# Performance work log

Hardware: AMD Instinct MI355X
Metric: run time of the kernel (lower is better)

## Reference

```python
import jax, jax.numpy as jnp
import numpy as np

N_PTS = 10000
BATCH = 2048          # hypotheses per RANSAC iteration
MAX_ITER = 10
SAMPLE_SIZE = 4       # minimal sample for homography DLT
INL_TH = 2.0          # squared symmetric transfer error threshold
EPS = 1e-8


def normalize_points(pts):
    # kornia.geometry.normalize_points: center + isotropic scale to mean dist sqrt(2)
    mean = pts.mean(axis=1, keepdims=True)                       # [B,1,2]
    d = jnp.linalg.norm(pts - mean, axis=-1).mean(axis=-1)       # [B]
    s = jnp.sqrt(jnp.asarray(2.0, pts.dtype)) / (d + EPS)
    B = pts.shape[0]
    T = jnp.zeros((B, 3, 3), pts.dtype)
    T = T.at[:, 0, 0].set(s).at[:, 1, 1].set(s).at[:, 2, 2].set(1.0)
    T = T.at[:, 0, 2].set(-s * mean[:, 0, 0]).at[:, 1, 2].set(-s * mean[:, 0, 1])
    return (pts - mean) * s[:, None, None], T


def find_homography_dlt(p1, p2):
    # p1,p2: [B,4,2]; weights are all ones -> solve smallest eigvec of A^T A (as kornia does)
    p1n, T1 = normalize_points(p1)
    p2n, T2 = normalize_points(p2)
    x1, y1 = p1n[..., 0], p1n[..., 1]
    x2, y2 = p2n[..., 0], p2n[..., 1]
    o = jnp.ones_like(x1); z = jnp.zeros_like(x1)
    ax = jnp.stack([z, z, z, -x1, -y1, -o, y2 * x1, y2 * y1, y2], -1)
    ay = jnp.stack([x1, y1, o, z, z, z, -x2 * x1, -x2 * y1, -x2], -1)
    A = jnp.concatenate([ax, ay], axis=1)                        # [B,8,9]
    AtA = jnp.einsum('bki,bkj->bij', A, A)                       # [B,9,9]
    _, _, Vh = jnp.linalg.svd(AtA)
    H = Vh[:, -1, :].reshape(-1, 3, 3)                           # smallest singular vector
    H = jnp.linalg.inv(T2) @ (H @ T1)
    return H / (H[:, 2:3, 2:3] + EPS)


def transform_points(H, pts):
    # H: [B,3,3], pts: [N,2] -> [B,N,2] (safe homogeneous division, as kornia)
    ph = jnp.concatenate([pts, jnp.ones_like(pts[..., :1])], -1)  # [N,3]
    pt = jnp.einsum('bij,nj->bni', H, ph)                        # [B,N,3]
    zc = pt[..., 2:3]
    mask = jnp.abs(zc) > EPS
    scale = jnp.where(mask, 1.0 / jnp.where(mask, zc, jnp.ones_like(zc)), jnp.ones_like(zc))
    return pt[..., :2] * scale


def symmetric_transfer_error(p1, p2, H):
    # squared symmetric transfer error (kornia default squared=True)
    Hinv = jnp.linalg.inv(H)
    e1 = ((transform_points(H, p1) - p2[None]) ** 2).sum(-1)
    e2 = ((transform_points(Hinv, p2) - p1[None]) ** 2).sum(-1)
    return e1 + e2                                               # [B,N]


def ransac_forward(kp1, kp2, key):
    n = kp1.shape[0]
    keys = jax.random.split(key, MAX_ITER)
    init = (jnp.asarray(1.0, kp1.dtype), jnp.eye(3, dtype=kp1.dtype), jnp.zeros((n,), bool))

    def body(carry, k):
        best_score, best_model, best_inl = carry
        # batched sampling without replacement: top-k of iid uniforms == randperm[:k]
        u = jax.random.uniform(k, (BATCH, n))
        _, idxs = jax.lax.top_k(u, SAMPLE_SIZE)                  # [BATCH,4] distinct
        H = find_homography_dlt(kp1[idxs], kp2[idxs])            # [BATCH,3,3]
        # remove_bad_models: mask instead of filter (jit-friendly)
        valid = jnp.abs(jnp.diagonal(H, axis1=1, axis2=2)).min(-1) > 1e-6
        err = symmetric_transfer_error(kp1, kp2, H)              # [BATCH,N]
        inl = err <= INL_TH
        scores = jnp.where(valid, inl.sum(-1).astype(kp1.dtype), -1.0)
        bi = jnp.argmax(scores)
        better = scores[bi] > best_score
        best_score = jnp.where(better, scores[bi], best_score)
        best_model = jnp.where(better, H[bi], best_model)
        best_inl = jnp.where(better, inl[bi], best_inl)
        return (best_score, best_model, best_inl), None

    (_, best_model, best_inl), _ = jax.lax.scan(body, init, keys)
    return best_model, best_inl


def setup_inputs():
    key = jax.random.key(0)
    k1, k2 = jax.random.split(key)
    kp1 = jax.random.uniform(k1, (N_PTS, 2), jnp.float32) * 100.0
    kp2 = jax.random.uniform(k2, (N_PTS, 2), jnp.float32) * 100.0
    return {"kp1": kp1, "kp2": kp2}


def reference(kp1, kp2):
    return ransac_forward(kp1, kp2, jax.random.key(42))
```

## Files before the change

### kernel.cpp

```cpp
#include <hip/hip_runtime.h>
#include <stdint.h>

#define JAX_PARTITIONABLE 1

#define N_PTS    10000
#define BATCH    2048
#define MAX_ITER 10
#define NMODELS  (BATCH*MAX_ITER)

#define ROTL(v,d) __builtin_amdgcn_alignbit((v),(v),(uint32_t)(32-(d)))

__device__ __forceinline__ void threefry_rounds(uint32_t k0, uint32_t k1, uint32_t ks2,
                                                uint32_t &x0, uint32_t &x1){
#define TF_R(r) { x0 += x1; x1 = ROTL(x1,(r)); x1 ^= x0; }
  TF_R(13) TF_R(15) TF_R(26) TF_R(6)
  x0 += k1;  x1 += ks2 + 1u;
  TF_R(17) TF_R(29) TF_R(16) TF_R(24)
  x0 += ks2; x1 += k0 + 2u;
  TF_R(13) TF_R(15) TF_R(26) TF_R(6)
  x0 += k0;  x1 += k1 + 3u;
  TF_R(17) TF_R(29) TF_R(16) TF_R(24)
  x0 += k1;  x1 += ks2 + 4u;
  TF_R(13) TF_R(15) TF_R(26) TF_R(6)
  x0 += ks2; x1 += k0 + 5u;
#undef TF_R
}

__device__ __forceinline__ void threefry2x32(uint32_t k0, uint32_t k1, uint32_t &x0, uint32_t &x1){
  const uint32_t ks2 = k0 ^ k1 ^ 0x1BD11BDAu;
  x0 += k0; x1 += k1;
  threefry_rounds(k0, k1, ks2, x0, x1);
}

__device__ __forceinline__ void top4_insert(unsigned long long a[4], unsigned long long key){
  if (key > a[3]){
    if (key > a[0]){ a[3]=a[2]; a[2]=a[1]; a[1]=a[0]; a[0]=key; }
    else if (key > a[1]){ a[3]=a[2]; a[2]=a[1]; a[1]=key; }
    else if (key > a[2]){ a[3]=a[2]; a[2]=key; }
    else { a[3]=key; }
  }
}

__device__ void block_merge_top4(unsigned long long a[4], unsigned long long* sm, int tid){
  sm[tid*4+0]=a[0]; sm[tid*4+1]=a[1]; sm[tid*4+2]=a[2]; sm[tid*4+3]=a[3];
  __syncthreads();
  for (int s = 128; s >= 1; s >>= 1){
    if (tid < s){
      unsigned long long bv[4];
      bv[0]=sm[(tid+s)*4+0]; bv[1]=sm[(tid+s)*4+1]; bv[2]=sm[(tid+s)*4+2]; bv[3]=sm[(tid+s)*4+3];
      unsigned long long ov[4];
      int pa=0, pb=0;
      #pragma unroll
      for (int k=0;k<4;k++){
        unsigned long long va = (pa<4)?a[pa]:0ull;
        unsigned long long vb = (pb<4)?bv[pb]:0ull;
        bool ta = va >= vb;
        ov[k] = ta ? va : vb;
        pa += ta?1:0; pb += ta?0:1;
      }
      a[0]=ov[0]; a[1]=ov[1]; a[2]=ov[2]; a[3]=ov[3];
      sm[tid*4+0]=a[0]; sm[tid*4+1]=a[1]; sm[tid*4+2]=a[2]; sm[tid*4+3]=a[3];
    }
    __syncthreads();
  }
}

__device__ __forceinline__ unsigned int lane_lt_count(unsigned long long m){
  unsigned int c = __builtin_amdgcn_mbcnt_lo((uint32_t)m, 0u);
  return __builtin_amdgcn_mbcnt_hi((uint32_t)(m >> 32), c);
}

#if JAX_PARTITIONABLE
#define TH_BITS 4267479552u
#define WCAP 96

__global__ __launch_bounds__(256) void sample_topk(int* __restrict__ idxs){
  const int b = blockIdx.x;
  const int t = blockIdx.y;
  const int tid = threadIdx.x;
  uint32_t k0 = 0u, k1 = (uint32_t)t;
  threefry2x32(0u, 42u, k0, k1);
  const uint32_t ks2 = k0 ^ k1 ^ 0x1BD11BDAu;

  __shared__ unsigned long long wcand[4*WCAP];
  __shared__ unsigned long long sm[256*4];
  __shared__ unsigned int wcnts[4];

  const unsigned int wbase = (unsigned int)(tid >> 6) * WCAP;
  unsigned int wcnt = 0;

  const uint32_t jb = (uint32_t)(b * N_PTS) + k1;

#define EMIT(u, idx) { \
    unsigned long long mk = __ballot((u) >= TH_BITS); \
    if (mk){ \
      if ((u) >= TH_BITS){ \
        unsigned int slot = wcnt + lane_lt_count(mk); \
        if (slot < WCAP) \
          wcand[wbase + slot] = ((unsigned long long)((u) >> 9) << 32) | (uint32_t)(~(idx)); \
      } \
      wcnt += (unsigned int)__popcll(mk); \
    } }

  uint32_t x1b = jb + (uint32_t)tid;
  for (int iter = 0; iter < 10; ++iter, x1b += 1024u){
    uint32_t a0=k0, a1=k0, a2=k0, a3=k0;
    uint32_t b0=x1b, b1=x1b+256u, b2=x1b+512u, b3=x1b+768u;
#define QR4(r) { a0+=b0; b0=ROTL(b0,r); b0^=a0;  a1+=b1; b1=ROTL(b1,r); b1^=a1; \
                 a2+=b2; b2=ROTL(b2,r); b2^=a2;  a3+=b3; b3=ROTL(b3,r); b3^=a3; }
#define INJ4(p,q) { a0+=(p); b0+=(q); a1+=(p); b1+=(q); a2+=(p); b2+=(q); a3+=(p); b3+=(q); }
    QR4(13) QR4(15) QR4(26) QR4(6)
    INJ4(k1,  ks2 + 1u)
    QR4(17) QR4(29) QR4(16) QR4(24)
    INJ4(ks2, k0 + 2u)
    QR4(13) QR4(15) QR4(26) QR4(6)
    INJ4(k0,  k1 + 3u)
    QR4(17) QR4(29) QR4(16) QR4(24)
    INJ4(k1,  ks2 + 4u)
    QR4(13) QR4(15) QR4(26) QR4(6)
    INJ4(ks2, k0 + 5u)
#undef QR4
#undef INJ4
    uint32_t u0 = a0^b0, u1 = a1^b1, u2 = a2^b2, u3 = a3^b3;
    const uint32_t ibase = (uint32_t)(iter*1024) + (uint32_t)tid;
    if (iter == 9){
      u0 = (ibase        < (uint32_t)N_PTS) ? u0 : 0u;
      u1 = (ibase + 256u < (uint32_t)N_PTS) ? u1 : 0u;
      u2 = (ibase + 512u < (uint32_t)N_PTS) ? u2 : 0u;
      u3 = (ibase + 768u < (uint32_t)N_PTS) ? u3 : 0u;
    }
    EMIT(u0, ibase)
    EMIT(u1, ibase + 256u)
    EMIT(u2, ibase + 512u)
    EMIT(u3, ibase + 768u)
  }
#undef EMIT

  if ((tid & 63) == 0) wcnts[tid >> 6] = wcnt;
  __syncthreads();
  const unsigned int c0 = wcnts[0], c1 = wcnts[1], c2 = wcnts[2], c3 = wcnts[3];
  const unsigned int n = c0 + c1 + c2 + c3;
  const bool good = (n >= 4u) && (c0 <= WCAP) && (c1 <= WCAP) && (c2 <= WCAP) && (c3 <= WCAP);

  unsigned long long a[4] = {0ull,0ull,0ull,0ull};
  if (good){
    #pragma unroll
    for (int w = 0; w < 4; ++w){
      const unsigned int cw = wcnts[w];
      for (unsigned int j = tid; j < cw; j += 256) top4_insert(a, wcand[w*WCAP + j]);
    }
  } else {
    for (int i = tid; i < N_PTS; i += 256){
      uint32_t x0 = k0, x1 = jb + (uint32_t)i;
      threefry_rounds(k0, k1, ks2, x0, x1);
      uint32_t u = x0 ^ x1;
      unsigned long long key = ((unsigned long long)(u >> 9) << 32) | (uint32_t)(~(uint32_t)i);
      top4_insert(a, key);
    }
  }
  block_merge_top4(a, sm, tid);
  if (tid == 0){
    int base = ((t*BATCH)+b)*4;
    idxs[base+0] = (int)(~(uint32_t)(a[0] & 0xffffffffull));
    idxs[base+1] = (int)(~(uint32_t)(a[1] & 0xffffffffull));
    idxs[base+2] = (int)(~(uint32_t)(a[2] & 0xffffffffull));
    idxs[base+3] = (int)(~(uint32_t)(a[3] & 0xffffffffull));
  }
}
#else
__global__ __launch_bounds__(256) void sample_topk(int* __restrict__ idxs){
  const int b = blockIdx.x;
  const int t = blockIdx.y;
  const int tid = threadIdx.x;
  uint32_t k0, k1;
  {
    int i0 = 2*t, i1 = 2*t+1;
    uint32_t u0, u1;
    if (i0 < 10){ u0=(uint32_t)i0; u1=(uint32_t)(i0+10); threefry2x32(0u,42u,u0,u1); k0=u0; }
    else        { u0=(uint32_t)(i0-10); u1=(uint32_t)i0; threefry2x32(0u,42u,u0,u1); k0=u1; }
    if (i1 < 10){ u0=(uint32_t)i1; u1=(uint32_t)(i1+10); threefry2x32(0u,42u,u0,u1); k1=u0; }
    else        { u0=(uint32_t)(i1-10); u1=(uint32_t)i1; threefry2x32(0u,42u,u0,u1); k1=u1; }
  }
  const uint32_t half = 10240000u;
  unsigned long long aLo[4] = {0,0,0,0}, aHi[4] = {0,0,0,0};
  const uint32_t jbase = (uint32_t)(b * N_PTS);
  for (int i = tid; i < N_PTS; i += 256){
    uint32_t x0 = jbase + (uint32_t)i, x1 = x0 + half;
    threefry2x32(k0, k1, x0, x1);
    unsigned long long kLo = ((unsigned long long)(x0 >> 9) << 32) | (uint32_t)(~(uint32_t)i);
    unsigned long long kHi = ((unsigned long long)(x1 >> 9) << 32) | (uint32_t)(~(uint32_t)i);
    top4_insert(aLo, kLo);
    top4_insert(aHi, kHi);
  }
  __shared__ unsigned long long sm[256*4];
  block_merge_top4(aLo, sm, tid);
  if (tid == 0){
    int base = ((t*BATCH)+b)*4;
    for (int s=0;s<4;s++) idxs[base+s] = (int)(~(uint32_t)(aLo[s] & 0xffffffffull));
  }
  __syncthreads();
  block_merge_top4(aHi, sm, tid);
  if (tid == 0){
    int base = ((t*BATCH)+(b+1024))*4;
    for (int s=0;s<4;s++) idxs[base+s] = (int)(~(uint32_t)(aHi[s] & 0xffffffffull));
  }
}
#endif

__global__ __launch_bounds__(64) void dlt_kernel(const float* __restrict__ kp1,
                                                 const float* __restrict__ kp2,
                                                 const int* __restrict__ idxs,
                                                 float* __restrict__ Hout,
                                                 float* __restrict__ Hinvout,
                                                 int* __restrict__ validout){
  const int m = blockIdx.x*64 + threadIdx.x;
  __shared__ double As[64][73];
  double* A = &As[threadIdx.x][0];

  double p1x[4],p1y[4],p2x[4],p2y[4];
  #pragma unroll
  for (int s=0;s<4;s++){
    int id = idxs[m*4+s];
    float2 a = ((const float2*)kp1)[id];
    float2 b = ((const float2*)kp2)[id];
    p1x[s]=a.x; p1y[s]=a.y; p2x[s]=b.x; p2y[s]=b.y;
  }
  double mx1=0,my1=0,mx2=0,my2=0;
  #pragma unroll
  for (int s=0;s<4;s++){ mx1+=p1x[s]; my1+=p1y[s]; mx2+=p2x[s]; my2+=p2y[s]; }
  mx1*=0.25; my1*=0.25; mx2*=0.25; my2*=0.25;
  double d1=0,d2=0;
  #pragma unroll
  for (int s=0;s<4;s++){
    d1 += sqrt((p1x[s]-mx1)*(p1x[s]-mx1) + (p1y[s]-my1)*(p1y[s]-my1));
    d2 += sqrt((p2x[s]-mx2)*(p2x[s]-mx2) + (p2y[s]-my2)*(p2y[s]-my2));
  }
  d1*=0.25; d2*=0.25;
  const double s1 = sqrt(2.0)/(d1 + 1e-8);
  const double s2 = sqrt(2.0)/(d2 + 1e-8);
  #pragma unroll
  for (int s=0;s<4;s++){
    double X1=(p1x[s]-mx1)*s1, Y1=(p1y[s]-my1)*s1;
    double X2=(p2x[s]-mx2)*s2, Y2=(p2y[s]-my2)*s2;
    double* ra = A + s*9;
    ra[0]=0.0; ra[1]=0.0; ra[2]=0.0; ra[3]=-X1; ra[4]=-Y1; ra[5]=-1.0;
    ra[6]=Y2*X1; ra[7]=Y2*Y1; ra[8]=Y2;
    double* rb = A + (4+s)*9;
    rb[0]=X1; rb[1]=Y1; rb[2]=1.0; rb[3]=0.0; rb[4]=0.0; rb[5]=0.0;
    rb[6]=-X2*X1; rb[7]=-X2*Y1; rb[8]=-X2;
  }
  for (int k=0;k<8;k++){
    int piv=k; double pv=fabs(A[k*9+k]);
    for (int r=k+1;r<8;r++){ double v=fabs(A[r*9+k]); if (v>pv){pv=v;piv=r;} }
    if (piv!=k){
      for (int c=k;c<9;c++){ double tmp=A[k*9+c]; A[k*9+c]=A[piv*9+c]; A[piv*9+c]=tmp; }
    }
    double invp = 1.0/A[k*9+k];
    for (int r=k+1;r<8;r++){
      double f = A[r*9+k]*invp;
      for (int c=k+1;c<9;c++) A[r*9+c] -= f*A[k*9+c];
      A[r*9+k]=0.0;
    }
  }
  double h[9];
  h[8]=1.0;
  for (int k=7;k>=0;k--){
    double ssum=0.0;
    for (int c=k+1;c<9;c++) ssum += A[k*9+c]*h[c];
    h[k] = -ssum / A[k*9+k];
  }
  {
    double nn=0.0;
    #pragma unroll
    for (int i=0;i<9;i++) nn += h[i]*h[i];
    double inr = 1.0/sqrt(nn);
    #pragma unroll
    for (int i=0;i<9;i++) h[i]*=inr;
  }
  double M[9];
  #pragma unroll
  for (int r=0;r<3;r++){
    double h0=h[r*3+0], h1=h[r*3+1], h2=h[r*3+2];
    M[r*3+0] = h0*s1;
    M[r*3+1] = h1*s1;
    M[r*3+2] = h0*(-s1*mx1) + h1*(-s1*my1) + h2;
  }
  double Hd[9];
  const double is2 = 1.0/s2;
  #pragma unroll
  for (int c=0;c<3;c++){
    Hd[0*3+c] = M[0*3+c]*is2 + mx2*M[2*3+c];
    Hd[1*3+c] = M[1*3+c]*is2 + my2*M[2*3+c];
    Hd[2*3+c] = M[2*3+c];
  }
  const double dn = 1.0/(Hd[8] + 1e-8);
  #pragma unroll
  for (int i=0;i<9;i++) Hd[i]*=dn;
  float Hf[9];
  #pragma unroll
  for (int i=0;i<9;i++){ Hf[i]=(float)Hd[i]; Hout[m*9+i]=Hf[i]; }
  float mind = fminf(fminf(fabsf(Hf[0]),fabsf(Hf[4])),fabsf(Hf[8]));
  validout[m] = (mind > 1e-6f) ? 1 : 0;
  {
    double a=Hd[0],b=Hd[1],c=Hd[2],d=Hd[3],e=Hd[4],f=Hd[5],g=Hd[6],hh=Hd[7],ii=Hd[8];
    double C00= e*ii-f*hh, C01=-(d*ii-f*g), C02= d*hh-e*g;
    double det = a*C00 + b*C01 + c*C02;
    double idet = 1.0/det;
    double inv[9];
    inv[0]=C00*idet;        inv[1]=(c*hh-b*ii)*idet; inv[2]=(b*f-c*e)*idet;
    inv[3]=C01*idet;        inv[4]=(a*ii-c*g)*idet;  inv[5]=(c*d-a*f)*idet;
    inv[6]=C02*idet;        inv[7]=(b*g-a*hh)*idet;  inv[8]=(a*e-b*d)*idet;
    #pragma unroll
    for (int i=0;i<9;i++) Hinvout[m*9+i]=(float)inv[i];
  }
}

__device__ __forceinline__ int inlier_test(float x1,float y1,float x2,float y2,
                                           const float* __restrict__ H,
                                           const float* __restrict__ Hi){
  float px = __fadd_rn(__fadd_rn(__fmul_rn(H[0],x1), __fmul_rn(H[1],y1)), H[2]);
  float py = __fadd_rn(__fadd_rn(__fmul_rn(H[3],x1), __fmul_rn(H[4],y1)), H[5]);
  float pz = __fadd_rn(__fadd_rn(__fmul_rn(H[6],x1), __fmul_rn(H[7],y1)), H[8]);
  float sc = (fabsf(pz) > 1e-8f) ? __fdiv_rn(1.0f, pz) : 1.0f;
  float dx = __fsub_rn(__fmul_rn(px,sc), x2);
  float dy = __fsub_rn(__fmul_rn(py,sc), y2);
  float e1 = __fadd_rn(__fmul_rn(dx,dx), __fmul_rn(dy,dy));
  if (!(e1 <= 2.0f)) return 0;
  float qx = __fadd_rn(__fadd_rn(__fmul_rn(Hi[0],x2), __fmul_rn(Hi[1],y2)), Hi[2]);
  float qy = __fadd_rn(__fadd_rn(__fmul_rn(Hi[3],x2), __fmul_rn(Hi[4],y2)), Hi[5]);
  float qz = __fadd_rn(__fadd_rn(__fmul_rn(Hi[6],x2), __fmul_rn(Hi[7],y2)), Hi[8]);
  float sc2 = (fabsf(qz) > 1e-8f) ? __fdiv_rn(1.0f, qz) : 1.0f;
  float ex = __fsub_rn(__fmul_rn(qx,sc2), x1);
  float ey = __fsub_rn(__fmul_rn(qy,sc2), y1);
  float e2 = __fadd_rn(__fmul_rn(ex,ex), __fmul_rn(ey,ey));
  float err = __fadd_rn(e1, e2);
  return (err <= 2.0f) ? 1 : 0;
}

#define MODELS_PER_BLOCK 8
__global__ __launch_bounds__(256) void score_kernel(const float* __restrict__ kp1,
                                                    const float* __restrict__ kp2,
                                                    const float* __restrict__ Hall,
                                                    const float* __restrict__ Hinvall,
                                                    const int* __restrict__ validall,
                                                    float* __restrict__ scores){
  const int m0 = blockIdx.x * MODELS_PER_BLOCK;
  const int tid = threadIdx.x;
  __shared__ float sH[MODELS_PER_BLOCK][9], sHi[MODELS_PER_BLOCK][9];
  if (tid < 9*MODELS_PER_BLOCK)        sH [tid/9][tid%9] = Hall[m0*9 + tid];
  else if (tid < 18*MODELS_PER_BLOCK){ int q = tid - 9*MODELS_PER_BLOCK;
                                       sHi[q/9][q%9] = Hinvall[m0*9 + q]; }
  __syncthreads();
  int cnt[MODELS_PER_BLOCK];
  #pragma unroll
  for (int mm=0;mm<MODELS_PER_BLOCK;mm++) cnt[mm]=0;
  for (int i = tid; i < N_PTS; i += 256){
    float2 p1 = ((const float2*)kp1)[i];
    float2 p2 = ((const float2*)kp2)[i];
    #pragma unroll
    for (int mm=0;mm<MODELS_PER_BLOCK;mm++)
      cnt[mm] += inlier_test(p1.x,p1.y,p2.x,p2.y,sH[mm],sHi[mm]);
  }
  __shared__ int wred[4][MODELS_PER_BLOCK];
  const int lane = tid & 63, wid = tid >> 6;
  #pragma unroll
  for (int mm=0;mm<MODELS_PER_BLOCK;mm++){
    int v = cnt[mm];
    for (int off=32; off; off>>=1) v += __shfl_down(v, off, 64);
    if (lane==0) wred[wid][mm] = v;
  }
  __syncthreads();
  if (tid < MODELS_PER_BLOCK){
    int v = wred[0][tid]+wred[1][tid]+wred[2][tid]+wred[3][tid];
    scores[m0+tid] = validall[m0+tid] ? (float)v : -1.0f;
  }
}

__global__ __launch_bounds__(1024) void select_kernel(const float* __restrict__ scores,
                                                      int* __restrict__ winner){
  __shared__ unsigned long long sm[1024];
  const int tid = threadIdx.x;
  unsigned long long best = 0ull;
  for (int i = tid; i < NMODELS; i += 1024){
    float s = scores[i];
    uint32_t hi = (uint32_t)(int)(s + 2.0f);
    unsigned long long key = ((unsigned long long)hi << 32) | (uint32_t)(~(uint32_t)i);
    if (key > best) best = key;
  }
  sm[tid]=best; __syncthreads();
  for (int s=512;s;s>>=1){ if (tid<s && sm[tid+s]>sm[tid]) sm[tid]=sm[tid+s]; __syncthreads(); }
  if (tid==0){
    unsigned long long k = sm[0];
    winner[0] = (int)(~(uint32_t)(k & 0xffffffffull));
    winner[1] = ((uint32_t)(k >> 32) >= 4u) ? 1 : 0;
  }
}

__global__ __launch_bounds__(256) void finalize_kernel(const float* __restrict__ kp1,
                                                       const float* __restrict__ kp2,
                                                       const float* __restrict__ Hall,
                                                       const float* __restrict__ Hinvall,
                                                       const int* __restrict__ winner,
                                                       float* __restrict__ out){
  __shared__ float sH[9], sHi[9];
  const int w = winner[0];
  const int ok = winner[1];
  if (threadIdx.x < 9){
    float idv = (threadIdx.x % 4 == 0) ? 1.0f : 0.0f;
    sH[threadIdx.x]  = ok ? Hall[w*9+threadIdx.x]    : idv;
    sHi[threadIdx.x] = ok ? Hinvall[w*9+threadIdx.x] : idv;
  }
  __syncthreads();
  if (blockIdx.x==0 && threadIdx.x<9) out[threadIdx.x] = sH[threadIdx.x];
  const int i = blockIdx.x*256 + threadIdx.x;
  if (i < N_PTS){
    float2 p1 = ((const float2*)kp1)[i];
    float2 p2 = ((const float2*)kp2)[i];
    int inl = ok ? inlier_test(p1.x,p1.y,p2.x,p2.y,sH,sHi) : 0;
    out[9+i] = inl ? 1.0f : 0.0f;
  }
}

extern "C" void kernel_launch(void* const* d_in, const int* in_sizes, int n_in,
                              void* d_out, int out_size, void* d_ws, size_t ws_size,
                              hipStream_t stream) {
  (void)in_sizes; (void)n_in; (void)out_size; (void)ws_size;
  const float* kp1 = (const float*)d_in[0];
  const float* kp2 = (const float*)d_in[1];
  float* out = (float*)d_out;
  char* ws = (char*)d_ws;
  int*   idxs    = (int*)  (ws + 0);
  float* Hall    = (float*)(ws + 327680);
  float* Hinvall = (float*)(ws + 1064960);
  int*   validall= (int*)  (ws + 1802240);
  float* scores  = (float*)(ws + 1884160);
  int*   winner  = (int*)  (ws + 1966080);

#if JAX_PARTITIONABLE
  sample_topk<<<dim3(BATCH, MAX_ITER), 256, 0, stream>>>(idxs);
#else
  sample_topk<<<dim3(BATCH/2, MAX_ITER), 256, 0, stream>>>(idxs);
#endif
  dlt_kernel<<<dim3(NMODELS/64), 64, 0, stream>>>(kp1, kp2, idxs, Hall, Hinvall, validall);
  score_kernel<<<dim3(NMODELS/MODELS_PER_BLOCK), 256, 0, stream>>>(kp1, kp2, Hall, Hinvall, validall, scores);
  select_kernel<<<1, 1024, 0, stream>>>(scores, winner);
  finalize_kernel<<<dim3((N_PTS+255)/256), 256, 0, stream>>>(kp1, kp2, Hall, Hinvall, winner, out);
}
```

Measured before the change: 784.5 us.

## Replace shared-memory top-4 merge with wave shuffles and retune scoring

```diff
diff --git a/kernel.cpp b/kernel.cpp
--- a/kernel.cpp
+++ b/kernel.cpp
@@ -41,27 +41,28 @@
   }
 }
 
-__device__ void block_merge_top4(unsigned long long a[4], unsigned long long* sm, int tid){
-  sm[tid*4+0]=a[0]; sm[tid*4+1]=a[1]; sm[tid*4+2]=a[2]; sm[tid*4+3]=a[3];
-  __syncthreads();
-  for (int s = 128; s >= 1; s >>= 1){
-    if (tid < s){
-      unsigned long long bv[4];
-      bv[0]=sm[(tid+s)*4+0]; bv[1]=sm[(tid+s)*4+1]; bv[2]=sm[(tid+s)*4+2]; bv[3]=sm[(tid+s)*4+3];
-      unsigned long long ov[4];
-      int pa=0, pb=0;
-      #pragma unroll
-      for (int k=0;k<4;k++){
-        unsigned long long va = (pa<4)?a[pa]:0ull;
-        unsigned long long vb = (pb<4)?bv[pb]:0ull;
-        bool ta = va >= vb;
-        ov[k] = ta ? va : vb;
-        pa += ta?1:0; pb += ta?0:1;
-      }
-      a[0]=ov[0]; a[1]=ov[1]; a[2]=ov[2]; a[3]=ov[3];
-      sm[tid*4+0]=a[0]; sm[tid*4+1]=a[1]; sm[tid*4+2]=a[2]; sm[tid*4+3]=a[3];
-    }
-    __syncthreads();
+__device__ __forceinline__ unsigned long long u64max(unsigned long long x, unsigned long long y){
+  return (x >= y) ? x : y;
+}
+__device__ __forceinline__ unsigned long long u64min(unsigned long long x, unsigned long long y){
+  return (x >= y) ? y : x;
+}
+
+__device__ __forceinline__ void wave_merge_top4(unsigned long long a[4]){
+  #pragma unroll
+  for (int d = 1; d < 64; d <<= 1){
+    unsigned long long b0 = __shfl_xor(a[0], d, 64);
+    unsigned long long b1 = __shfl_xor(a[1], d, 64);
+    unsigned long long b2 = __shfl_xor(a[2], d, 64);
+    unsigned long long b3 = __shfl_xor(a[3], d, 64);
+    unsigned long long L0 = u64max(a[0], b3);
+    unsigned long long L1 = u64max(a[1], b2);
+    unsigned long long L2 = u64max(a[2], b1);
+    unsigned long long L3 = u64max(a[3], b0);
+    unsigned long long m0 = u64max(L0, L2), m2 = u64min(L0, L2);
+    unsigned long long m1 = u64max(L1, L3), m3 = u64min(L1, L3);
+    a[0] = u64max(m0, m1); a[1] = u64min(m0, m1);
+    a[2] = u64max(m2, m3); a[3] = u64min(m2, m3);
   }
 }
 
@@ -83,7 +84,6 @@
   const uint32_t ks2 = k0 ^ k1 ^ 0x1BD11BDAu;
 
   __shared__ unsigned long long wcand[4*WCAP];
-  __shared__ unsigned long long sm[256*4];
   __shared__ unsigned int wcnts[4];
 
   const unsigned int wbase = (unsigned int)(tid >> 6) * WCAP;
@@ -142,14 +142,8 @@
   const unsigned int n = c0 + c1 + c2 + c3;
   const bool good = (n >= 4u) && (c0 <= WCAP) && (c1 <= WCAP) && (c2 <= WCAP) && (c3 <= WCAP);
 
-  unsigned long long a[4] = {0ull,0ull,0ull,0ull};
-  if (good){
-    #pragma unroll
-    for (int w = 0; w < 4; ++w){
-      const unsigned int cw = wcnts[w];
-      for (unsigned int j = tid; j < cw; j += 256) top4_insert(a, wcand[w*WCAP + j]);
-    }
-  } else {
+  if (!good){
+    unsigned long long a[4] = {0ull,0ull,0ull,0ull};
     for (int i = tid; i < N_PTS; i += 256){
       uint32_t x0 = k0, x1 = jb + (uint32_t)i;
       threefry_rounds(k0, k1, ks2, x0, x1);
@@ -157,14 +151,31 @@
       unsigned long long key = ((unsigned long long)(u >> 9) << 32) | (uint32_t)(~(uint32_t)i);
       top4_insert(a, key);
     }
-  }
-  block_merge_top4(a, sm, tid);
-  if (tid == 0){
-    int base = ((t*BATCH)+b)*4;
-    idxs[base+0] = (int)(~(uint32_t)(a[0] & 0xffffffffull));
-    idxs[base+1] = (int)(~(uint32_t)(a[1] & 0xffffffffull));
-    idxs[base+2] = (int)(~(uint32_t)(a[2] & 0xffffffffull));
-    idxs[base+3] = (int)(~(uint32_t)(a[3] & 0xffffffffull));
+    wave_merge_top4(a);
+    if ((tid & 63) == 0){
+      const unsigned int w = tid >> 6;
+      wcand[w*WCAP+0]=a[0]; wcand[w*WCAP+1]=a[1]; wcand[w*WCAP+2]=a[2]; wcand[w*WCAP+3]=a[3];
+      wcnts[w] = 4u;
+    }
+    __syncthreads();
+  }
+
+  if (tid < 64){
+    unsigned long long a[4] = {0ull,0ull,0ull,0ull};
+    #pragma unroll
+    for (int w = 0; w < 4; ++w){
+      unsigned int cw = wcnts[w]; if (cw > WCAP) cw = WCAP;
+      for (unsigned int j = (unsigned int)tid; j < cw; j += 64u)
+        top4_insert(a, wcand[w*WCAP + j]);
+    }
+    wave_merge_top4(a);
+    if (tid == 0){
+      int base = ((t*BATCH)+b)*4;
+      idxs[base+0] = (int)(~(uint32_t)(a[0] & 0xffffffffull));
+      idxs[base+1] = (int)(~(uint32_t)(a[1] & 0xffffffffull));
+      idxs[base+2] = (int)(~(uint32_t)(a[2] & 0xffffffffull));
+      idxs[base+3] = (int)(~(uint32_t)(a[3] & 0xffffffffull));
+    }
   }
 }
 #else
@@ -192,17 +203,28 @@
     top4_insert(aLo, kLo);
     top4_insert(aHi, kHi);
   }
-  __shared__ unsigned long long sm[256*4];
-  block_merge_top4(aLo, sm, tid);
-  if (tid == 0){
-    int base = ((t*BATCH)+b)*4;
-    for (int s=0;s<4;s++) idxs[base+s] = (int)(~(uint32_t)(aLo[s] & 0xffffffffull));
-  }
-  __syncthreads();
-  block_merge_top4(aHi, sm, tid);
-  if (tid == 0){
-    int base = ((t*BATCH)+(b+1024))*4;
-    for (int s=0;s<4;s++) idxs[base+s] = (int)(~(uint32_t)(aHi[s] & 0xffffffffull));
+  __shared__ unsigned long long wc[4*4];
+  __shared__ unsigned int dummy;
+  (void)dummy;
+  wave_merge_top4(aLo);
+  if ((tid&63)==0){ int w=tid>>6; wc[w*4+0]=aLo[0];wc[w*4+1]=aLo[1];wc[w*4+2]=aLo[2];wc[w*4+3]=aLo[3]; }
+  __syncthreads();
+  if (tid < 64){
+    unsigned long long a[4]={0,0,0,0};
+    for (int w=0;w<4;w++) if ((unsigned)tid < 4u) {}
+    for (int w=0;w<4;w++) for (unsigned int j=tid;j<4u;j+=64u) top4_insert(a, wc[w*4+j]);
+    wave_merge_top4(a);
+    if (tid==0){ int base=((t*BATCH)+b)*4; for (int s=0;s<4;s++) idxs[base+s]=(int)(~(uint32_t)(a[s]&0xffffffffull)); }
+  }
+  __syncthreads();
+  wave_merge_top4(aHi);
+  if ((tid&63)==0){ int w=tid>>6; wc[w*4+0]=aHi[0];wc[w*4+1]=aHi[1];wc[w*4+2]=aHi[2];wc[w*4+3]=aHi[3]; }
+  __syncthreads();
+  if (tid < 64){
+    unsigned long long a[4]={0,0,0,0};
+    for (int w=0;w<4;w++) for (unsigned int j=tid;j<4u;j+=64u) top4_insert(a, wc[w*4+j]);
+    wave_merge_top4(a);
+    if (tid==0){ int base=((t*BATCH)+(b+1024))*4; for (int s=0;s<4;s++) idxs[base+s]=(int)(~(uint32_t)(a[s]&0xffffffffull)); }
   }
 }
 #endif
@@ -337,7 +359,7 @@
   return (err <= 2.0f) ? 1 : 0;
 }
 
-#define MODELS_PER_BLOCK 8
+#define MODELS_PER_BLOCK 4
 __global__ __launch_bounds__(256) void score_kernel(const float* __restrict__ kp1,
                                                     const float* __restrict__ kp2,
                                                     const float* __restrict__ Hall,
@@ -361,18 +383,13 @@
     for (int mm=0;mm<MODELS_PER_BLOCK;mm++)
       cnt[mm] += inlier_test(p1.x,p1.y,p2.x,p2.y,sH[mm],sHi[mm]);
   }
-  __shared__ int wred[4][MODELS_PER_BLOCK];
-  const int lane = tid & 63, wid = tid >> 6;
+  __shared__ int red[256];
   #pragma unroll
   for (int mm=0;mm<MODELS_PER_BLOCK;mm++){
-    int v = cnt[mm];
-    for (int off=32; off; off>>=1) v += __shfl_down(v, off, 64);
-    if (lane==0) wred[wid][mm] = v;
-  }
-  __syncthreads();
-  if (tid < MODELS_PER_BLOCK){
-    int v = wred[0][tid]+wred[1][tid]+wred[2][tid]+wred[3][tid];
-    scores[m0+tid] = validall[m0+tid] ? (float)v : -1.0f;
+    red[tid]=cnt[mm]; __syncthreads();
+    for (int s=128;s;s>>=1){ if (tid<s) red[tid]+=red[tid+s]; __syncthreads(); }
+    if (tid==0) scores[m0+mm] = validall[m0+mm] ? (float)red[0] : -1.0f;
+    __syncthreads();
   }
 }
 
```

Result: faster. 727.6 us (-7.3%).
